# Kernel optimization log

Hardware: AMD Instinct MI355X
Metric: run time of the kernel (lower is better)

## Reference

```python
import jax, jax.numpy as jnp
import numpy as np

T, N, K = 32, 1024, 15
IN_CH, CONV_CH, HEADS, ODIM = 64, 64, 2, 50
D = CONV_CH // 2  # GRU hidden size (conv_ch // 2)


def setup_inputs():
    ks = jax.random.split(jax.random.key(0), 24)
    x = jax.random.normal(ks[0], (T, N, IN_CH), jnp.float32)
    # fixed-degree adjacency: exactly K distinct non-self sources per (t, target)
    rnd = jax.random.uniform(ks[1], (T, N, N - 1))
    off = jnp.argsort(rnd, axis=-1)[..., :K]            # [T,N,K] in [0, N-2]
    tgt = jnp.arange(N)[None, :, None]
    src = (tgt + 1 + off) % N                           # distinct sources != target
    edge = jnp.zeros((T, N, N), jnp.int32).at[jnp.arange(T)[:, None, None], src, tgt].set(1)

    def lin(k, fi, fo):
        return jax.random.normal(k, (fi, fo), jnp.float32) / float(np.sqrt(fi))

    p, i = {}, 2
    for nm, fi, c in (("g1", IN_CH, CONV_CH), ("g2", CONV_CH, D), ("r1", D, CONV_CH), ("f1", D, CONV_CH)):
        p[nm + "_Wl"] = lin(ks[i], fi, HEADS * c)
        p[nm + "_bl"] = jnp.zeros((HEADS * c,), jnp.float32)
        p[nm + "_Wr"] = lin(ks[i + 1], fi, HEADS * c)
        p[nm + "_br"] = jnp.zeros((HEADS * c,), jnp.float32)
        p[nm + "_att"] = jax.random.normal(ks[i + 2], (HEADS, c), jnp.float32) / float(np.sqrt(c))
        p[nm + "_b"] = jnp.zeros((c,), jnp.float32)
        i += 3
    for nm in ("gru0", "gru1"):
        p[nm + "_Wih"] = lin(ks[i], D, 3 * D).T         # [3D, D], PyTorch layout
        p[nm + "_Whh"] = lin(ks[i + 1], D, 3 * D).T
        p[nm + "_bih"] = jnp.zeros((3 * D,), jnp.float32)
        p[nm + "_bhh"] = jnp.zeros((3 * D,), jnp.float32)
        i += 2
    p["rec2_W"] = lin(ks[i], CONV_CH, IN_CH)
    p["rec2_b"] = jnp.zeros((IN_CH,), jnp.float32)
    p["rec3_W"] = lin(ks[i + 1], IN_CH, ODIM)
    p["rec3_b"] = jnp.zeros((ODIM,), jnp.float32)
    p["fore3_W"] = lin(ks[i + 2], IN_CH, ODIM)
    p["fore3_b"] = jnp.zeros((ODIM,), jnp.float32)
    return {"x": x, "edge": edge, **p}


def _gat(x, srcs, prm):
    # GATv2Conv, concat=False: mean over heads; srcs: [K+1, N] sources per target
    Wl, bl, Wr, br, att, bias = prm
    H, C = att.shape
    gl = (x @ Wl + bl).reshape(-1, H, C)                # source-side lin_l
    gr = (x @ Wr + br).reshape(-1, H, C)                # target-side lin_r
    gsrc = gl[srcs]                                     # [K+1, N, H, C] gather
    e = jax.nn.leaky_relu(gsrc + gr[None], 0.2)
    logits = jnp.einsum('knhc,hc->knh', e, att)
    alpha = jax.nn.softmax(logits, axis=0)              # softmax over neighbors per target
    return jnp.einsum('knh,knhc->nhc', alpha, gsrc).mean(axis=1) + bias


def _gat_t(xs, srcs, prm):
    return jax.vmap(lambda a, s: _gat(a, s, prm))(xs, srcs)


def _gru(xs, Wih, Whh, bih, bhh):
    # PyTorch GRU cell math, zero initial state, seq-first [T, N, D]
    h0 = jnp.zeros((xs.shape[1], Whh.shape[1]), xs.dtype)

    def step(h, xt):
        gi = xt @ Wih.T + bih
        gh = h @ Whh.T + bhh
        ir, iz, inew = jnp.split(gi, 3, axis=-1)
        hr, hz, hn = jnp.split(gh, 3, axis=-1)
        r = jax.nn.sigmoid(ir + hr)
        z = jax.nn.sigmoid(iz + hz)
        n = jnp.tanh(inew + r * hn)
        hnew = (1.0 - z) * n + z * h
        return hnew, hnew

    _, ys = jax.lax.scan(step, h0, xs)
    return ys


def _forward(x, edge, g1, g2, r1, f1, gru0, gru1, rec2_W, rec2_b, rec3_W, rec3_b, fore3_W, fore3_b):
    # recover the K in-edges per target (edge[t, src, tgt] == 1), then append self loops
    srcs = jnp.argsort(-edge, axis=1)[:, :K, :]         # [T, K, N]
    self_idx = jnp.broadcast_to(jnp.arange(N)[None, None, :], (edge.shape[0], 1, N))
    srcs = jnp.concatenate([srcs, self_idx.astype(srcs.dtype)], axis=1)  # [T, K+1, N]

    out = jax.nn.elu(_gat_t(x, srcs, g1))               # dropout is a no-op in eval
    out2 = jax.nn.elu(_gat_t(out, srcs, g2))
    E = _gru(out2, *gru0)
    E = _gru(E, *gru1)

    rec = jax.nn.elu(_gat_t(E[1:], srcs[1:], r1))       # timesteps 1..T-1
    rec = jnp.tanh(rec @ rec2_W + rec2_b)
    recon = rec @ rec3_W + rec3_b

    fc = jax.nn.elu(_gat_t(E[:-1], srcs[:-1], f1))      # timesteps 0..T-2
    fc = jnp.tanh(fc @ rec2_W + rec2_b)                 # original code reuses reconstruct2 here
    forecast = fc @ fore3_W + fore3_b
    return recon, forecast, E


def reference(x, edge, g1_Wl, g1_bl, g1_Wr, g1_br, g1_att, g1_b,
              g2_Wl, g2_bl, g2_Wr, g2_br, g2_att, g2_b,
              r1_Wl, r1_bl, r1_Wr, r1_br, r1_att, r1_b,
              f1_Wl, f1_bl, f1_Wr, f1_br, f1_att, f1_b,
              gru0_Wih, gru0_Whh, gru0_bih, gru0_bhh,
              gru1_Wih, gru1_Whh, gru1_bih, gru1_bhh,
              rec2_W, rec2_b, rec3_W, rec3_b, fore3_W, fore3_b):
    return _forward(x, edge,
                    (g1_Wl, g1_bl, g1_Wr, g1_br, g1_att, g1_b),
                    (g2_Wl, g2_bl, g2_Wr, g2_br, g2_att, g2_b),
                    (r1_Wl, r1_bl, r1_Wr, r1_br, r1_att, r1_b),
                    (f1_Wl, f1_bl, f1_Wr, f1_br, f1_att, f1_b),
                    (gru0_Wih, gru0_Whh, gru0_bih, gru0_bhh),
                    (gru1_Wih, gru1_Whh, gru1_bih, gru1_bhh),
                    rec2_W, rec2_b, rec3_W, rec3_b, fore3_W, fore3_b)
```

## Files before the change

### kernel.cpp

```cpp
#include <hip/hip_runtime.h>
#include <math.h>

static constexpr int Tt = 32;
static constexpr int Nn = 1024;
static constexpr int KN = 16;
static constexpr float LOG2E = 1.44269504f;

template <int M>
__device__ __forceinline__ float lane_xor(float v) {
    if constexpr (M == 1)
        return __int_as_float(__builtin_amdgcn_mov_dpp(__float_as_int(v), 0xB1, 0xF, 0xF, true));
    else if constexpr (M == 2)
        return __int_as_float(__builtin_amdgcn_mov_dpp(__float_as_int(v), 0x4E, 0xF, 0xF, true));
    else
        return __shfl_xor(v, M);
}
__device__ __forceinline__ constexpr int rev4(int k) {
    return ((k & 1) << 3) | ((k & 2) << 1) | ((k & 4) >> 1) | ((k & 8) >> 3);
}
template <int NV, int M>
__device__ __forceinline__ void fstage(float* p, int lane) {
#pragma unroll
    for (int k2 = 0; k2 < NV / 2; ++k2) {
        float a_ = p[k2], b_ = p[k2 + NV / 2];
        float t_ = (lane & M) ? a_ : b_;
        float r_ = lane_xor<M>(t_);
        p[k2] = ((lane & M) ? b_ : a_) + r_;
    }
}
__device__ __forceinline__ float fold16(float* p, int lane) {
    fstage<16, 1>(p, lane); fstage<8, 2>(p, lane);
    fstage<4, 4>(p, lane);  fstage<2, 8>(p, lane);
    return p[0];
}
__device__ __forceinline__ float rsum16(float x) {
    x += lane_xor<1>(x); x += lane_xor<2>(x);
    x += lane_xor<4>(x); x += lane_xor<8>(x);
    return x;
}
__device__ __forceinline__ float bperm_alpha(float v, int pbase, int r4) {
    return __int_as_float(__builtin_amdgcn_ds_bpermute(pbase + (r4 << 2), __float_as_int(v)));
}
__device__ __forceinline__ float elu(float x) {
    return x > 0.0f ? x : (__builtin_amdgcn_exp2f(LOG2E * x) - 1.0f);
}
__device__ __forceinline__ float fast_tanh(float x) {
    return 1.0f - 2.0f * __builtin_amdgcn_rcpf(1.0f + __builtin_amdgcn_exp2f((2.0f * LOG2E) * x));
}

__global__ __launch_bounds__(1024) void k_srcs(const int* __restrict__ edge,
                                               int* __restrict__ srcs)
{
    __shared__ int cnt[64];
    const int t    = blockIdx.x >> 4;
    const int tgt0 = (blockIdx.x & 15) << 6;
    const int x = threadIdx.x & 15;
    const int y = threadIdx.x >> 4;
    if (threadIdx.x < 64) cnt[threadIdx.x] = 0;
    __syncthreads();

    const int c0 = 4 * x;
    const int s0 = y * 16;
    const int* e = edge + (size_t)t * Nn * Nn + tgt0 + c0;

    for (int i0 = 0; i0 < 16; i0 += 8) {
        int4 v[8];
#pragma unroll
        for (int j = 0; j < 8; ++j)
            v[j] = *reinterpret_cast<const int4*>(e + (size_t)(s0 + i0 + j) * Nn);
#pragma unroll
        for (int j = 0; j < 8; ++j) {
            const int s = s0 + i0 + j;
            if (v[j].x) { int sl = atomicAdd(&cnt[c0],     1); if (sl < KN - 1) srcs[((size_t)t * Nn + tgt0 + c0)     * KN + sl] = s; }
            if (v[j].y) { int sl = atomicAdd(&cnt[c0 + 1], 1); if (sl < KN - 1) srcs[((size_t)t * Nn + tgt0 + c0 + 1) * KN + sl] = s; }
            if (v[j].z) { int sl = atomicAdd(&cnt[c0 + 2], 1); if (sl < KN - 1) srcs[((size_t)t * Nn + tgt0 + c0 + 2) * KN + sl] = s; }
            if (v[j].w) { int sl = atomicAdd(&cnt[c0 + 3], 1); if (sl < KN - 1) srcs[((size_t)t * Nn + tgt0 + c0 + 3) * KN + sl] = s; }
        }
    }
    if (threadIdx.x < 64)
        srcs[((size_t)t * Nn + tgt0 + threadIdx.x) * KN + (KN - 1)] = tgt0 + threadIdx.x;
}

template <int FI, int FO>
__global__ __launch_bounds__(256) void k_lin2t(
    const float* __restrict__ X,
    const float* __restrict__ Wl, const float* __restrict__ bl,
    const float* __restrict__ Wr, const float* __restrict__ br,
    float* __restrict__ Yl, float* __restrict__ Yr, int rows)
{
    constexpr int HC = FO / 2;
    constexpr int RG = 256 / HC;
    constexpr int R  = 8;
    constexpr int BR = RG * R;
    constexpr int F4 = FI / 4;
    __shared__ float xs[BR][FI];

    const int tid  = threadIdx.x;
    const int c    = tid % HC;
    const int g    = tid / HC;
    const int row0 = blockIdx.x * BR;

#pragma unroll
    for (int idx = tid; idx < BR * F4; idx += 256) {
        int r = idx / F4, q = idx % F4;
        reinterpret_cast<float4*>(&xs[r][0])[q] =
            reinterpret_cast<const float4*>(X + (size_t)(row0 + r) * FI)[q];
    }
    __syncthreads();

    float al0[R], al1[R], ar0[R], ar1[R];
    const float bl0 = bl[c], bl1 = bl[c + HC], br0 = br[c], br1 = br[c + HC];
#pragma unroll
    for (int r = 0; r < R; ++r) { al0[r] = bl0; al1[r] = bl1; ar0[r] = br0; ar1[r] = br1; }

    const int rb = g * R;
#pragma unroll
    for (int i0 = 0; i0 < FI; i0 += 4) {
        float4 xv[R];
#pragma unroll
        for (int r = 0; r < R; ++r)
            xv[r] = *reinterpret_cast<const float4*>(&xs[rb + r][i0]);
#pragma unroll
        for (int j = 0; j < 4; ++j) {
            const float wl0 = Wl[(i0 + j) * FO + c];
            const float wl1 = Wl[(i0 + j) * FO + c + HC];
            const float wr0 = Wr[(i0 + j) * FO + c];
            const float wr1 = Wr[(i0 + j) * FO + c + HC];
#pragma unroll
            for (int r = 0; r < R; ++r) {
                const float xx = (&xv[r].x)[j];
                al0[r] = fmaf(xx, wl0, al0[r]);
                al1[r] = fmaf(xx, wl1, al1[r]);
                ar0[r] = fmaf(xx, wr0, ar0[r]);
                ar1[r] = fmaf(xx, wr1, ar1[r]);
            }
        }
    }
#pragma unroll
    for (int r = 0; r < R; ++r) {
        const size_t ro = (size_t)(row0 + rb + r) * FO;
        reinterpret_cast<float2*>(Yl + ro)[c] = make_float2(al0[r], al1[r]);
        reinterpret_cast<float2*>(Yr + ro)[c] = make_float2(ar0[r], ar1[r]);
    }
}

__global__ __launch_bounds__(256) void k_lin2td(
    const float* __restrict__ E,
    const float* __restrict__ WlA, const float* __restrict__ blA,
    const float* __restrict__ WrA, const float* __restrict__ brA,
    float* __restrict__ YlA, float* __restrict__ YrA,
    const float* __restrict__ WlB, const float* __restrict__ blB,
    const float* __restrict__ WrB, const float* __restrict__ brB,
    float* __restrict__ YlB, float* __restrict__ YrB)
{
    constexpr int FI = 32, FO = 128, HC = 64, R = 8, BR = 32, F4 = FI / 4;
    __shared__ float xs[BR][FI];

    int bid = blockIdx.x;
    const bool second = bid >= 992;
    if (second) bid -= 992;

    const float* X  = second ? E   : (E + (size_t)Nn * FI);
    const float* Wl = second ? WlB : WlA;
    const float* bl = second ? blB : blA;
    const float* Wr = second ? WrB : WrA;
    const float* br = second ? brB : brA;
    float* Yl = second ? YlB : YlA;
    float* Yr = second ? YrB : YrA;

    const int tid  = threadIdx.x;
    const int c    = tid % HC;
    const int g    = tid / HC;
    const int row0 = bid * BR;

#pragma unroll
    for (int idx = tid; idx < BR * F4; idx += 256) {
        int r = idx / F4, q = idx % F4;
        reinterpret_cast<float4*>(&xs[r][0])[q] =
            reinterpret_cast<const float4*>(X + (size_t)(row0 + r) * FI)[q];
    }
    __syncthreads();

    float al0[R], al1[R], ar0[R], ar1[R];
    const float bl0 = bl[c], bl1 = bl[c + HC], br0 = br[c], br1 = br[c + HC];
#pragma unroll
    for (int r = 0; r < R; ++r) { al0[r] = bl0; al1[r] = bl1; ar0[r] = br0; ar1[r] = br1; }

    const int rb = g * R;
#pragma unroll
    for (int i0 = 0; i0 < FI; i0 += 4) {
        float4 xv[R];
#pragma unroll
        for (int r = 0; r < R; ++r)
            xv[r] = *reinterpret_cast<const float4*>(&xs[rb + r][i0]);
#pragma unroll
        for (int j = 0; j < 4; ++j) {
            const float wl0 = Wl[(i0 + j) * FO + c];
            const float wl1 = Wl[(i0 + j) * FO + c + HC];
            const float wr0 = Wr[(i0 + j) * FO + c];
            const float wr1 = Wr[(i0 + j) * FO + c + HC];
#pragma unroll
            for (int r = 0; r < R; ++r) {
                const float xx = (&xv[r].x)[j];
                al0[r] = fmaf(xx, wl0, al0[r]);
                al1[r] = fmaf(xx, wl1, al1[r]);
                ar0[r] = fmaf(xx, wr0, ar0[r]);
                ar1[r] = fmaf(xx, wr1, ar1[r]);
            }
        }
    }
#pragma unroll
    for (int r = 0; r < R; ++r) {
        const size_t ro = (size_t)(row0 + rb + r) * FO;
        reinterpret_cast<float2*>(Yl + ro)[c] = make_float2(al0[r], al1[r]);
        reinterpret_cast<float2*>(Yr + ro)[c] = make_float2(ar0[r], ar1[r]);
    }
}

__global__ __launch_bounds__(192) void k_lin96(
    const float* __restrict__ X, const float* __restrict__ W,
    const float* __restrict__ b, float* __restrict__ Y)
{
    __shared__ float wT[32 * 97];
    __shared__ float xs[16][32];

    const int tid = threadIdx.y * 96 + threadIdx.x;
    const int row0 = blockIdx.x * 16;

    for (int idx = tid; idx < 3072; idx += 192) {
        int c = idx >> 5, i = idx & 31;
        wT[i * 97 + c] = W[idx];
    }
    for (int idx = tid; idx < 128; idx += 192)
        reinterpret_cast<float4*>(xs)[idx] =
            reinterpret_cast<const float4*>(X + (size_t)row0 * 32)[idx];
    __syncthreads();

    const int c  = threadIdx.x;
    const int rb = threadIdx.y * 8;
    float acc[8];
    const float bc = b[c];
#pragma unroll
    for (int r = 0; r < 8; ++r) acc[r] = bc;

#pragma unroll
    for (int i = 0; i < 32; ++i) {
        const float w = wT[i * 97 + c];
#pragma unroll
        for (int r = 0; r < 8; ++r)
            acc[r] = fmaf(xs[rb + r][i], w, acc[r]);
    }
#pragma unroll
    for (int r = 0; r < 8; ++r)
        Y[(size_t)(row0 + rb + r) * 96 + c] = acc[r];
}

__global__ __launch_bounds__(64) void k_gru1(
    const float* __restrict__ gi, const float* __restrict__ Whh,
    const float* __restrict__ bhh, float* __restrict__ E)
{
    const int d    = threadIdx.x & 31;
    const int node = blockIdx.x * 2 + (threadIdx.x >> 5);

    float wr_[32], wz_[32], wn_[32];
#pragma unroll
    for (int q = 0; q < 8; ++q) {
        *reinterpret_cast<float4*>(&wr_[q * 4]) =
            reinterpret_cast<const float4*>(Whh + (size_t)d * 32)[q];
        *reinterpret_cast<float4*>(&wz_[q * 4]) =
            reinterpret_cast<const float4*>(Whh + (size_t)(32 + d) * 32)[q];
        *reinterpret_cast<float4*>(&wn_[q * 4]) =
            reinterpret_cast<const float4*>(Whh + (size_t)(64 + d) * 32)[q];
    }
    const float br_ = bhh[d], bz_ = bhh[32 + d], bn_ = bhh[64 + d];

    size_t base = (size_t)node * 96 + d;
    float gr = gi[base], gz = gi[base + 32], gn = gi[base + 64];

    float h = 0.0f;
    for (int t = 0; t < Tt; ++t) {
        float grn = 0.f, gzn = 0.f, gnn = 0.f;
        if (t < Tt - 1) {
            const size_t nb = ((size_t)(t + 1) * Nn + node) * 96 + d;
            grn = gi[nb]; gzn = gi[nb + 32]; gnn = gi[nb + 64];
        }
        float ar = br_, az = bz_, an = bn_;
#pragma unroll
        for (int i = 0; i < 32; ++i) {
            const float hv = __shfl(h, i, 32);
            ar = fmaf(wr_[i], hv, ar);
            az = fmaf(wz_[i], hv, az);
            an = fmaf(wn_[i], hv, an);
        }
        const float r = __builtin_amdgcn_rcpf(1.0f + __builtin_amdgcn_exp2f(-LOG2E * (gr + ar)));
        const float z = __builtin_amdgcn_rcpf(1.0f + __builtin_amdgcn_exp2f(-LOG2E * (gz + az)));
        const float nn2 = fast_tanh(gn + r * an);
        h = (1.0f - z) * nn2 + z * h;
        E[((size_t)t * Nn + node) * 32 + d] = h;
        gr = grn; gz = gzn; gn = gnn;
    }
}

__device__ __forceinline__ void gat64_pair_body(
    const float* __restrict__ gl, const float* __restrict__ gr,
    const int* __restrict__ srcs, const float* __restrict__ att,
    const float* __restrict__ bias, int wv, int lane,
    float* __restrict__ out)
{
    const int tgt = 2 * wv + (lane >> 5);
    const int t = tgt >> 10;
    const int n = tgt & (Nn - 1);
    const int c = lane & 31;

    const float2* grrow = reinterpret_cast<const float2*>(gr) + (size_t)tgt * 64;
    const float2 grl0 = grrow[c];
    const float2 grl1 = grrow[32 + c];
    const float a00 = att[c],      a01 = att[32 + c];
    const float a10 = att[64 + c], a11 = att[96 + c];

    const int4* sp = reinterpret_cast<const int4*>(srcs + ((size_t)t * Nn + n) * KN);
    const int4 sA = sp[0], sB = sp[1], sC = sp[2], sD = sp[3];
    int s[KN] = {sA.x, sA.y, sA.z, sA.w, sB.x, sB.y, sB.z, sB.w,
                 sC.x, sC.y, sC.z, sC.w, sD.x, sD.y, sD.z, sD.w};

    const float2* glt = reinterpret_cast<const float2*>(gl) + ((size_t)t * Nn * 64);

    float2 g0[KN], g1[KN];
    float p0[KN], p1[KN];
#pragma unroll
    for (int k = 0; k < KN; ++k) {
        const unsigned ro = (unsigned)(s[k] << 6);
        g0[k] = glt[ro | c];
        g1[k] = glt[ro | (32 + c)];
        float e00 = g0[k].x + grl0.x; e00 = fmaxf(e00, 0.2f * e00);
        float e01 = g1[k].x + grl1.x; e01 = fmaxf(e01, 0.2f * e01);
        float e10 = g0[k].y + grl0.y; e10 = fmaxf(e10, 0.2f * e10);
        float e11 = g1[k].y + grl1.y; e11 = fmaxf(e11, 0.2f * e11);
        p0[k] = fmaf(e01, a01, e00 * a00);
        p1[k] = fmaf(e11, a11, e10 * a10);
    }
    float lo0 = fold16(p0, lane); lo0 += lane_xor<16>(lo0);
    float lo1 = fold16(p1, lane); lo1 += lane_xor<16>(lo1);

    const float e0 = __builtin_amdgcn_exp2f(LOG2E * lo0);
    const float e1 = __builtin_amdgcn_exp2f(LOG2E * lo1);
    const float A0 = e0 * __builtin_amdgcn_rcpf(rsum16(e0));
    const float A1 = e1 * __builtin_amdgcn_rcpf(rsum16(e1));

    const int pbase = (lane & 32) << 2;
    float acc00 = 0.0f, acc01 = 0.0f, acc10 = 0.0f, acc11 = 0.0f;
#pragma unroll
    for (int k = 0; k < KN; ++k) {
        const float b0 = bperm_alpha(A0, pbase, rev4(k));
        const float b1 = bperm_alpha(A1, pbase, rev4(k));
        acc00 = fmaf(b0, g0[k].x, acc00);
        acc01 = fmaf(b0, g1[k].x, acc01);
        acc10 = fmaf(b1, g0[k].y, acc10);
        acc11 = fmaf(b1, g1[k].y, acc11);
    }
    float r0 = 0.5f * (acc00 + acc10) + bias[c];
    float r1 = 0.5f * (acc01 + acc11) + bias[32 + c];
    out[(size_t)tgt * 64 + c]      = elu(r0);
    out[(size_t)tgt * 64 + 32 + c] = elu(r1);
}

__global__ __launch_bounds__(256, 4) void k_gat64p(
    const float* __restrict__ gl, const float* __restrict__ gr,
    const int* __restrict__ srcs, const float* __restrict__ att,
    const float* __restrict__ bias, float* __restrict__ out, int pairs)
{
    const int lane = threadIdx.x & 63;
    const int w = threadIdx.x >> 6;
    const int gridB = pairs >> 2;
    const int chunk = gridB >> 3;
    const int bid = blockIdx.x;
    const int lb = (bid & 7) * chunk + (bid >> 3);
    const int wv = lb * 4 + w;
    gat64_pair_body(gl, gr, srcs, att, bias, wv, lane, out);
}

__global__ __launch_bounds__(256, 4) void k_gat64p2(
    const float* __restrict__ glA, const float* __restrict__ grA,
    const int* __restrict__ srcsA, const float* __restrict__ attA,
    const float* __restrict__ biasA, float* __restrict__ outA,
    const float* __restrict__ glB, const float* __restrict__ grB,
    const int* __restrict__ srcsB, const float* __restrict__ attB,
    const float* __restrict__ biasB, float* __restrict__ outB)
{
    constexpr int pairs = (Tt - 1) * Nn / 2;
    constexpr int gridH = pairs >> 2;
    constexpr int chunk = gridH >> 3;

    int bid = blockIdx.x;
    const bool second = bid >= gridH;
    if (second) bid -= gridH;

    const float* gl   = second ? glB   : glA;
    const float* gr   = second ? grB   : grA;
    const int*   srcs = second ? srcsB : srcsA;
    const float* att  = second ? attB  : attA;
    const float* bias = second ? biasB : biasA;
    float*       out  = second ? outB  : outA;

    const int lane = threadIdx.x & 63;
    const int w = threadIdx.x >> 6;
    const int lb = (bid & 7) * chunk + (bid >> 3);
    const int wv = lb * 4 + w;
    gat64_pair_body(gl, gr, srcs, att, bias, wv, lane, out);
}

__global__ __launch_bounds__(256, 4) void k_gat32(
    const float* __restrict__ gl, const float* __restrict__ gr,
    const int* __restrict__ srcs, const float* __restrict__ att,
    const float* __restrict__ bias, float* __restrict__ out, int waves)
{
    const int lane = threadIdx.x & 63;
    const int w = threadIdx.x >> 6;
    const int gridB = waves >> 2;
    const int chunk = gridB >> 3;
    const int bid = blockIdx.x;
    const int lb = (bid & 7) * chunk + (bid >> 3);
    const int wv = lb * 4 + w;
    const int tgt = 2 * wv + (lane >> 5);
    const int t = tgt >> 10;
    const int n = tgt & (Nn - 1);
    const int c = lane & 31;

    const float2 grl = reinterpret_cast<const float2*>(gr + (size_t)tgt * 64)[c];
    const float a0 = att[c], a1 = att[32 + c];

    const int4* sp = reinterpret_cast<const int4*>(srcs + ((size_t)t * Nn + n) * KN);
    const int4 sA = sp[0], sB = sp[1], sC = sp[2], sD = sp[3];
    int s[KN] = {sA.x, sA.y, sA.z, sA.w, sB.x, sB.y, sB.z, sB.w,
                 sC.x, sC.y, sC.z, sC.w, sD.x, sD.y, sD.z, sD.w};

    const float2* glt = reinterpret_cast<const float2*>(gl) + ((size_t)t * Nn * 32);

    float2 g[KN];
    float p0[KN], p1[KN];
#pragma unroll
    for (int k = 0; k < KN; ++k) {
        g[k] = glt[(unsigned)((s[k] << 5) | c)];
        float e0 = g[k].x + grl.x; e0 = fmaxf(e0, 0.2f * e0);
        float e1 = g[k].y + grl.y; e1 = fmaxf(e1, 0.2f * e1);
        p0[k] = e0 * a0; p1[k] = e1 * a1;
    }
    float lo0 = fold16(p0, lane); lo0 += lane_xor<16>(lo0);
    float lo1 = fold16(p1, lane); lo1 += lane_xor<16>(lo1);

    const float e0 = __builtin_amdgcn_exp2f(LOG2E * lo0);
    const float e1 = __builtin_amdgcn_exp2f(LOG2E * lo1);
    const float A0 = e0 * __builtin_amdgcn_rcpf(rsum16(e0));
    const float A1 = e1 * __builtin_amdgcn_rcpf(rsum16(e1));

    const int pbase = (lane & 32) << 2;
    float acc0 = 0.0f, acc1 = 0.0f;
#pragma unroll
    for (int k = 0; k < KN; ++k) {
        const float b0 = bperm_alpha(A0, pbase, rev4(k));
        const float b1 = bperm_alpha(A1, pbase, rev4(k));
        acc0 = fmaf(b0, g[k].x, acc0);
        acc1 = fmaf(b1, g[k].y, acc1);
    }
    float res = 0.5f * (acc0 + acc1) + bias[c];
    out[(size_t)tgt * 32 + c] = elu(res);
}

__global__ __launch_bounds__(256) void k_head2(
    const float* __restrict__ inA, const float* __restrict__ W3A,
    const float* __restrict__ b3A, float* __restrict__ outA,
    const float* __restrict__ inB, const float* __restrict__ W3B,
    const float* __restrict__ b3B, float* __restrict__ outB,
    const float* __restrict__ W2, const float* __restrict__ b2)
{
    __shared__ float xs[32][64];
    __shared__ float tmp[32][64];

    int bid = blockIdx.x;
    const bool second = bid >= 992;
    if (second) bid -= 992;

    const float* in  = second ? inB  : inA;
    const float* W3  = second ? W3B  : W3A;
    const float* b3  = second ? b3B  : b3A;
    float*       out = second ? outB : outA;

    const int c = threadIdx.x;
    const int g = threadIdx.y;
    const int tid = g * 64 + c;
    const int row0 = bid * 32;

    for (int idx = tid; idx < 32 * 16; idx += 256) {
        int r = idx >> 4, q = idx & 15;
        reinterpret_cast<float4*>(&xs[r][0])[q] =
            reinterpret_cast<const float4*>(in + (size_t)(row0 + r) * 64)[q];
    }
    __syncthreads();

    const int rb = g * 8;
    float acc[8];
    const float bc = b2[c];
#pragma unroll
    for (int r = 0; r < 8; ++r) acc[r] = bc;
#pragma unroll
    for (int i = 0; i < 64; ++i) {
        const float w2 = W2[i * 64 + c];
#pragma unroll
        for (int r = 0; r < 8; ++r)
            acc[r] = fmaf(xs[rb + r][i], w2, acc[r]);
    }
#pragma unroll
    for (int r = 0; r < 8; ++r) tmp[rb + r][c] = fast_tanh(acc[r]);

    const int cc = c < 50 ? c : 0;
    float a[8];
    const float b3c = b3[cc];
#pragma unroll
    for (int r = 0; r < 8; ++r) a[r] = b3c;
#pragma unroll
    for (int j = 0; j < 64; ++j) {
        const float w3 = W3[j * 50 + cc];
#pragma unroll
        for (int r = 0; r < 8; ++r)
            a[r] = fmaf(tmp[rb + r][j], w3, a[r]);
    }
    if (c < 50) {
#pragma unroll
        for (int r = 0; r < 8; ++r)
            out[(size_t)(row0 + rb + r) * 50 + c] = a[r];
    }
}

extern "C" void kernel_launch(void* const* d_in, const int* in_sizes, int n_in,
                              void* d_out, int out_size, void* d_ws, size_t ws_size,
                              hipStream_t stream)
{
    const float* x    = (const float*)d_in[0];
    const int*   edge = (const int*)d_in[1];

    const float *g1_Wl = (const float*)d_in[2],  *g1_bl = (const float*)d_in[3];
    const float *g1_Wr = (const float*)d_in[4],  *g1_br = (const float*)d_in[5];
    const float *g1_att= (const float*)d_in[6],  *g1_b  = (const float*)d_in[7];
    const float *g2_Wl = (const float*)d_in[8],  *g2_bl = (const float*)d_in[9];
    const float *g2_Wr = (const float*)d_in[10], *g2_br = (const float*)d_in[11];
    const float *g2_att= (const float*)d_in[12], *g2_b  = (const float*)d_in[13];
    const float *r1_Wl = (const float*)d_in[14], *r1_bl = (const float*)d_in[15];
    const float *r1_Wr = (const float*)d_in[16], *r1_br = (const float*)d_in[17];
    const float *r1_att= (const float*)d_in[18], *r1_b  = (const float*)d_in[19];
    const float *f1_Wl = (const float*)d_in[20], *f1_bl = (const float*)d_in[21];
    const float *f1_Wr = (const float*)d_in[22], *f1_br = (const float*)d_in[23];
    const float *f1_att= (const float*)d_in[24], *f1_b  = (const float*)d_in[25];
    const float *gru0_Wih = (const float*)d_in[26], *gru0_Whh = (const float*)d_in[27];
    const float *gru0_bih = (const float*)d_in[28], *gru0_bhh = (const float*)d_in[29];
    const float *gru1_Wih = (const float*)d_in[30], *gru1_Whh = (const float*)d_in[31];
    const float *gru1_bih = (const float*)d_in[32], *gru1_bhh = (const float*)d_in[33];
    const float *rec2_W = (const float*)d_in[34], *rec2_b = (const float*)d_in[35];
    const float *rec3_W = (const float*)d_in[36], *rec3_b = (const float*)d_in[37];
    const float *fore3_W= (const float*)d_in[38], *fore3_b= (const float*)d_in[39];

    char* ws = (char*)d_ws;
    int*   srcs = (int*)ws;
    float* buf1 = (float*)(ws + (4u << 20));
    float* buf2 = buf1 + (size_t)32768 * 128;
    float* buf3 = buf2 + (size_t)32768 * 128;
    float* buf4 = buf3 + (size_t)32768 * 128;
    float* buf5 = buf4 + (size_t)32768 * 128;
    float* buf6 = buf5 + (size_t)32768 * 64;

    float* recon = (float*)d_out;
    float* fore  = recon + (size_t)31 * 1024 * 50;
    float* E     = fore  + (size_t)31 * 1024 * 50;

    k_srcs<<<Tt * 16, 1024, 0, stream>>>(edge, srcs);

    k_lin2t<64, 128><<<1024, 256, 0, stream>>>(x, g1_Wl, g1_bl, g1_Wr, g1_br, buf1, buf2, 32768);
    k_gat64p<<<4096, 256, 0, stream>>>(buf1, buf2, srcs, g1_att, g1_b, buf5, 16384);

    k_lin2t<64, 64><<<512, 256, 0, stream>>>(buf5, g2_Wl, g2_bl, g2_Wr, g2_br, buf1, buf2, 32768);
    k_gat32<<<4096, 256, 0, stream>>>(buf1, buf2, srcs, g2_att, g2_b, buf6, 16384);

    k_lin96<<<2048, dim3(96, 2), 0, stream>>>(buf6, gru0_Wih, gru0_bih, buf1);
    k_gru1<<<512, 64, 0, stream>>>(buf1, gru0_Whh, gru0_bhh, buf5);
    k_lin96<<<2048, dim3(96, 2), 0, stream>>>(buf5, gru1_Wih, gru1_bih, buf2);
    k_gru1<<<512, 64, 0, stream>>>(buf2, gru1_Whh, gru1_bhh, E);

    k_lin2td<<<1984, 256, 0, stream>>>(E,
        r1_Wl, r1_bl, r1_Wr, r1_br, buf1, buf2,
        f1_Wl, f1_bl, f1_Wr, f1_br, buf3, buf4);

    k_gat64p2<<<7936, 256, 0, stream>>>(
        buf1, buf2, srcs + (size_t)KN * Nn, r1_att, r1_b, buf5,
        buf3, buf4, srcs,                   f1_att, f1_b, buf6);
    k_head2<<<1984, dim3(64, 4), 0, stream>>>(
        buf5, rec3_W, rec3_b, recon,
        buf6, fore3_W, fore3_b, fore,
        rec2_W, rec2_b);

    (void)in_sizes; (void)n_in; (void)out_size; (void)ws_size;
}
```

Baseline: 240.6 us.

## Fuse both GRU layers and input projections into one recurrent kernel

Replaces the two input-projection kernels and the two recurrent kernels with a single kernel that computes both GRU layers step by step, doing the input projections inline. Weights are staged in shared memory (48KB per 64-thread block) instead of registers. This removes three launches and the global round-trips for the gate-input and intermediate hidden buffers. In exchange, the serial per-step work roughly quadruples (input and hidden matvecs for two layers), occupancy is limited by shared memory, and the 32-step dependency chain is lengthened.

```diff
diff --git a/kernel.cpp b/kernel.cpp
--- a/kernel.cpp
+++ b/kernel.cpp
@@ -44,6 +44,9 @@
 __device__ __forceinline__ float elu(float x) {
     return x > 0.0f ? x : (__builtin_amdgcn_exp2f(LOG2E * x) - 1.0f);
 }
+__device__ __forceinline__ float fast_sigmoid(float x) {
+    return __builtin_amdgcn_rcpf(1.0f + __builtin_amdgcn_exp2f(-LOG2E * x));
+}
 __device__ __forceinline__ float fast_tanh(float x) {
     return 1.0f - 2.0f * __builtin_amdgcn_rcpf(1.0f + __builtin_amdgcn_exp2f((2.0f * LOG2E) * x));
 }
@@ -217,87 +220,86 @@
     }
 }
 
-__global__ __launch_bounds__(192) void k_lin96(
-    const float* __restrict__ X, const float* __restrict__ W,
-    const float* __restrict__ b, float* __restrict__ Y)
-{
-    __shared__ float wT[32 * 97];
-    __shared__ float xs[16][32];
-
-    const int tid = threadIdx.y * 96 + threadIdx.x;
-    const int row0 = blockIdx.x * 16;
-
-    for (int idx = tid; idx < 3072; idx += 192) {
-        int c = idx >> 5, i = idx & 31;
-        wT[i * 97 + c] = W[idx];
-    }
-    for (int idx = tid; idx < 128; idx += 192)
-        reinterpret_cast<float4*>(xs)[idx] =
-            reinterpret_cast<const float4*>(X + (size_t)row0 * 32)[idx];
+__global__ __launch_bounds__(64) void k_gru2f(
+    const float* __restrict__ x,
+    const float* __restrict__ Wih0, const float* __restrict__ bih0,
+    const float* __restrict__ Whh0, const float* __restrict__ bhh0,
+    const float* __restrict__ Wih1, const float* __restrict__ bih1,
+    const float* __restrict__ Whh1, const float* __restrict__ bhh1,
+    float* __restrict__ E)
+{
+    __shared__ float u0[3072], w0[3072], u1[3072], w1[3072];
+    const int tid = threadIdx.x;
+
+    for (int idx = tid; idx < 768; idx += 64) {
+        const int i4 = idx / 96;
+        const int j  = idx % 96;
+        const float4 a = *reinterpret_cast<const float4*>(Wih0 + j * 32 + i4 * 4);
+        const float4 b = *reinterpret_cast<const float4*>(Whh0 + j * 32 + i4 * 4);
+        const float4 cc = *reinterpret_cast<const float4*>(Wih1 + j * 32 + i4 * 4);
+        const float4 dd = *reinterpret_cast<const float4*>(Whh1 + j * 32 + i4 * 4);
+#pragma unroll
+        for (int q = 0; q < 4; ++q) {
+            const int ii = i4 * 4 + q;
+            u0[ii * 96 + j] = (&a.x)[q];
+            w0[ii * 96 + j] = (&b.x)[q];
+            u1[ii * 96 + j] = (&cc.x)[q];
+            w1[ii * 96 + j] = (&dd.x)[q];
+        }
+    }
+    const int d    = tid & 31;
+    const int node = blockIdx.x * 2 + (tid >> 5);
+    const float bi0r = bih0[d], bi0z = bih0[32 + d], bi0n = bih0[64 + d];
+    const float bh0r = bhh0[d], bh0z = bhh0[32 + d], bh0n = bhh0[64 + d];
+    const float bi1r = bih1[d], bi1z = bih1[32 + d], bi1n = bih1[64 + d];
+    const float bh1r = bhh1[d], bh1z = bhh1[32 + d], bh1n = bhh1[64 + d];
     __syncthreads();
 
-    const int c  = threadIdx.x;
-    const int rb = threadIdx.y * 8;
-    float acc[8];
-    const float bc = b[c];
-#pragma unroll
-    for (int r = 0; r < 8; ++r) acc[r] = bc;
-
-#pragma unroll
-    for (int i = 0; i < 32; ++i) {
-        const float w = wT[i * 97 + c];
-#pragma unroll
-        for (int r = 0; r < 8; ++r)
-            acc[r] = fmaf(xs[rb + r][i], w, acc[r]);
-    }
-#pragma unroll
-    for (int r = 0; r < 8; ++r)
-        Y[(size_t)(row0 + rb + r) * 96 + c] = acc[r];
-}
-
-__global__ __launch_bounds__(64) void k_gru1(
-    const float* __restrict__ gi, const float* __restrict__ Whh,
-    const float* __restrict__ bhh, float* __restrict__ E)
-{
-    const int d    = threadIdx.x & 31;
-    const int node = blockIdx.x * 2 + (threadIdx.x >> 5);
-
-    float wr_[32], wz_[32], wn_[32];
-#pragma unroll
-    for (int q = 0; q < 8; ++q) {
-        *reinterpret_cast<float4*>(&wr_[q * 4]) =
-            reinterpret_cast<const float4*>(Whh + (size_t)d * 32)[q];
-        *reinterpret_cast<float4*>(&wz_[q * 4]) =
-            reinterpret_cast<const float4*>(Whh + (size_t)(32 + d) * 32)[q];
-        *reinterpret_cast<float4*>(&wn_[q * 4]) =
-            reinterpret_cast<const float4*>(Whh + (size_t)(64 + d) * 32)[q];
-    }
-    const float br_ = bhh[d], bz_ = bhh[32 + d], bn_ = bhh[64 + d];
-
-    size_t base = (size_t)node * 96 + d;
-    float gr = gi[base], gz = gi[base + 32], gn = gi[base + 64];
-
-    float h = 0.0f;
+    float h0 = 0.0f, h1 = 0.0f;
+    float xv = x[(size_t)node * 32 + d];
     for (int t = 0; t < Tt; ++t) {
-        float grn = 0.f, gzn = 0.f, gnn = 0.f;
-        if (t < Tt - 1) {
-            const size_t nb = ((size_t)(t + 1) * Nn + node) * 96 + d;
-            grn = gi[nb]; gzn = gi[nb + 32]; gnn = gi[nb + 64];
+        float xnx = 0.0f;
+        if (t < Tt - 1)
+            xnx = x[((size_t)(t + 1) * Nn + node) * 32 + d];
+
+        float gr = bi0r, gz = bi0z, gn = bi0n;
+        float ar = bh0r, az = bh0z, an = bh0n;
+#pragma unroll
+        for (int i = 0; i < 32; ++i) {
+            const float xi = __shfl(xv, i, 32);
+            const float hv = __shfl(h0, i, 32);
+            gr = fmaf(xi, u0[i * 96 + d], gr);
+            gz = fmaf(xi, u0[i * 96 + 32 + d], gz);
+            gn = fmaf(xi, u0[i * 96 + 64 + d], gn);
+            ar = fmaf(hv, w0[i * 96 + d], ar);
+            az = fmaf(hv, w0[i * 96 + 32 + d], az);
+            an = fmaf(hv, w0[i * 96 + 64 + d], an);
         }
-        float ar = br_, az = bz_, an = bn_;
+        float r = fast_sigmoid(gr + ar);
+        float z = fast_sigmoid(gz + az);
+        float n2 = fast_tanh(gn + r * an);
+        h0 = (1.0f - z) * n2 + z * h0;
+
+        gr = bi1r; gz = bi1z; gn = bi1n;
+        ar = bh1r; az = bh1z; an = bh1n;
 #pragma unroll
         for (int i = 0; i < 32; ++i) {
-            const float hv = __shfl(h, i, 32);
-            ar = fmaf(wr_[i], hv, ar);
-            az = fmaf(wz_[i], hv, az);
-            an = fmaf(wn_[i], hv, an);
+            const float xi = __shfl(h0, i, 32);
+            const float hv = __shfl(h1, i, 32);
+            gr = fmaf(xi, u1[i * 96 + d], gr);
+            gz = fmaf(xi, u1[i * 96 + 32 + d], gz);
+            gn = fmaf(xi, u1[i * 96 + 64 + d], gn);
+            ar = fmaf(hv, w1[i * 96 + d], ar);
+            az = fmaf(hv, w1[i * 96 + 32 + d], az);
+            an = fmaf(hv, w1[i * 96 + 64 + d], an);
         }
-        const float r = __builtin_amdgcn_rcpf(1.0f + __builtin_amdgcn_exp2f(-LOG2E * (gr + ar)));
-        const float z = __builtin_amdgcn_rcpf(1.0f + __builtin_amdgcn_exp2f(-LOG2E * (gz + az)));
-        const float nn2 = fast_tanh(gn + r * an);
-        h = (1.0f - z) * nn2 + z * h;
-        E[((size_t)t * Nn + node) * 32 + d] = h;
-        gr = grn; gz = gzn; gn = gnn;
+        r = fast_sigmoid(gr + ar);
+        z = fast_sigmoid(gz + az);
+        n2 = fast_tanh(gn + r * an);
+        h1 = (1.0f - z) * n2 + z * h1;
+
+        E[((size_t)t * Nn + node) * 32 + d] = h1;
+        xv = xnx;
     }
 }
 
@@ -579,10 +581,9 @@
     k_lin2t<64, 64><<<512, 256, 0, stream>>>(buf5, g2_Wl, g2_bl, g2_Wr, g2_br, buf1, buf2, 32768);
     k_gat32<<<4096, 256, 0, stream>>>(buf1, buf2, srcs, g2_att, g2_b, buf6, 16384);
 
-    k_lin96<<<2048, dim3(96, 2), 0, stream>>>(buf6, gru0_Wih, gru0_bih, buf1);
-    k_gru1<<<512, 64, 0, stream>>>(buf1, gru0_Whh, gru0_bhh, buf5);
-    k_lin96<<<2048, dim3(96, 2), 0, stream>>>(buf5, gru1_Wih, gru1_bih, buf2);
-    k_gru1<<<512, 64, 0, stream>>>(buf2, gru1_Whh, gru1_bhh, E);
+    k_gru2f<<<512, 64, 0, stream>>>(buf6,
+        gru0_Wih, gru0_bih, gru0_Whh, gru0_bhh,
+        gru1_Wih, gru1_bih, gru1_Whh, gru1_bhh, E);
 
     k_lin2td<<<1984, 256, 0, stream>>>(E,
         r1_Wl, r1_bl, r1_Wr, r1_br, buf1, buf2,
```

Result: slower. 308.3 us (+28.1%).
